# Kernel tuning notes

Measured on AMD Instinct MI355X. Metric: run time of the kernel, lower is better.

## Reference

```python
import jax, jax.numpy as jnp
import numpy as np

N = 50000
E = 800000
F_IN = 128
HID = 64
HEADS = 4
NUM_TYPES = 1
NEG_SLOPE = 0.2


def setup_inputs() -> dict:
    key = jax.random.key(0)
    ks = jax.random.split(key, 20)
    s = 0.05
    inp = {
        "node_features": jax.random.normal(ks[0], (N, F_IN), jnp.float32),
        "node_types": jax.random.randint(ks[1], (N,), 0, NUM_TYPES, jnp.int32),
        "edge_index": jax.random.randint(ks[2], (2, E), 0, N, jnp.int32),
        # params
        "type_emb": jax.random.normal(ks[3], (NUM_TYPES, HID), jnp.float32) * s,
        "proj_w": jax.random.normal(ks[4], (F_IN, HID), jnp.float32) * s,
        "proj_b": jnp.zeros((HID,), jnp.float32),
        # GAT layer 0: in=64 -> heads*64, concat=True
        "lin_w0": jax.random.normal(ks[5], (HID, HEADS * HID), jnp.float32) * s,
        "att_src0": jax.random.normal(ks[6], (HEADS, HID), jnp.float32) * s,
        "att_dst0": jax.random.normal(ks[7], (HEADS, HID), jnp.float32) * s,
        "bias0": jnp.zeros((HEADS * HID,), jnp.float32),
        "ln_g0": jnp.ones((HEADS * HID,), jnp.float32),
        "ln_b0": jnp.zeros((HEADS * HID,), jnp.float32),
        # GAT layer 1: in=256 -> heads*64, concat=False (mean over heads)
        "lin_w1": jax.random.normal(ks[8], (HEADS * HID, HEADS * HID), jnp.float32) * s,
        "att_src1": jax.random.normal(ks[9], (HEADS, HID), jnp.float32) * s,
        "att_dst1": jax.random.normal(ks[10], (HEADS, HID), jnp.float32) * s,
        "bias1": jnp.zeros((HID,), jnp.float32),
        "ln_g1": jnp.ones((HID,), jnp.float32),
        "ln_b1": jnp.zeros((HID,), jnp.float32),
    }
    return inp


def _layer_norm(x, g, b, eps=1e-5):
    mu = jnp.mean(x, axis=-1, keepdims=True)
    var = jnp.mean(jnp.square(x - mu), axis=-1, keepdims=True)
    return (x - mu) * jax.lax.rsqrt(var + eps) * g + b


def _gat_conv(x, src, dst, lin_w, att_src, att_dst, bias, concat):
    # PyG GATConv: linear -> per-edge additive attention -> segment softmax over
    # incoming edges -> weighted scatter-sum. Self-loops already in src/dst.
    n = x.shape[0]
    H, C = att_src.shape
    h = (x @ lin_w).reshape(n, H, C)            # [N,H,C]
    a_s = jnp.sum(h * att_src[None], axis=-1)   # [N,H]
    a_d = jnp.sum(h * att_dst[None], axis=-1)   # [N,H]
    a = jax.nn.leaky_relu(a_s[src] + a_d[dst], NEG_SLOPE)  # [E,H]
    m = jax.ops.segment_max(a, dst, num_segments=n)
    e = jnp.exp(a - m[dst])
    z = jax.ops.segment_sum(e, dst, num_segments=n)
    alpha = e / z[dst]                           # [E,H]
    msg = h[src] * alpha[..., None]              # [E,H,C]
    out = jax.ops.segment_sum(msg, dst, num_segments=n)  # [N,H,C]
    if concat:
        out = out.reshape(n, H * C)
    else:
        out = out.mean(axis=1)
    return out + bias


def reference(node_features, node_types, edge_index,
              type_emb, proj_w, proj_b,
              lin_w0, att_src0, att_dst0, bias0, ln_g0, ln_b0,
              lin_w1, att_src1, att_dst1, bias1, ln_g1, ln_b1):
    n = node_features.shape[0]
    # add self loops (PyG GATConv default add_self_loops=True)
    loop = jnp.arange(n, dtype=edge_index.dtype)
    src = jnp.concatenate([edge_index[0], loop])
    dst = jnp.concatenate([edge_index[1], loop])

    x = node_features @ proj_w + proj_b + type_emb[node_types]  # [N,64]

    # layer 0: no residual (i == 0)
    x = _gat_conv(x, src, dst, lin_w0, att_src0, att_dst0, bias0, concat=True)
    x = jax.nn.relu(_layer_norm(x, ln_g0, ln_b0))  # [N,256]; dropout = identity (eval)

    # layer 1: residual shape [N,256] != output [N,64] -> residual skipped
    x = _gat_conv(x, src, dst, lin_w1, att_src1, att_dst1, bias1, concat=False)
    x = jax.nn.relu(_layer_norm(x, ln_g1, ln_b1))  # [N,64]
    return x
```

## Files before the change

### kernel.cpp

```cpp
#include <hip/hip_runtime.h>


#define BLK 256
#define FB  768

typedef __bf16 bf16x8 __attribute__((ext_vector_type(8)));
typedef __bf16 bf16x4 __attribute__((ext_vector_type(4)));
typedef float  f32x4  __attribute__((ext_vector_type(4)));


__device__ __forceinline__ void pack_body(const float* __restrict__ w,
                                          __bf16* __restrict__ wp,
                                          int K, int NC, int idx) {
  const int tot = (K >> 3) * NC;
  if (idx >= tot) return;
  int g = idx / NC, c = idx - g * NC;
#pragma unroll
  for (int j = 0; j < 8; ++j)
    wp[(size_t)idx * 8 + j] = (__bf16)w[(g * 8 + j) * NC + c];
}


__global__ __launch_bounds__(BLK) void k_prep(
    const float* __restrict__ pw, const float* __restrict__ w0,
    const float* __restrict__ w1, __bf16* __restrict__ pwp,
    __bf16* __restrict__ w0p, __bf16* __restrict__ w1p,
    int* __restrict__ cnt, int* __restrict__ sidx, int n, int nchunks) {
  int b = blockIdx.x;
  const int t = threadIdx.x;
  if (b < nchunks) {
    int i = b * BLK + t;
    if (i < n) { cnt[i] = 1; sidx[(size_t)i << 6] = i; }
    return;
  }
  b -= nchunks;
  if (b < 4)  { pack_body(pw, pwp, 128, 64,  b * BLK + t); return; }
  b -= 4;
  if (b < 8)  { pack_body(w0, w0p, 64, 256,  b * BLK + t); return; }
  b -= 8;
  pack_body(w1, w1p, 256, 256, b * BLK + t);
}

__global__ __launch_bounds__(BLK) void k_fill_projlin0(
    const int* __restrict__ src, const int* __restrict__ dst,
    int* __restrict__ cnt, int* __restrict__ sidx, int E,
    const float* __restrict__ nf, const int* __restrict__ types,
    const __bf16* __restrict__ pwp, const float* __restrict__ pb,
    const float* __restrict__ emb,
    const __bf16* __restrict__ w0p,
    const float* __restrict__ asrc0, const float* __restrict__ adst0,
    __bf16* __restrict__ H, float* __restrict__ as_, float* __restrict__ ad_,
    int n) {
  __shared__ __bf16 xt[64][72];
  if (blockIdx.x < FB) {
    const int st = FB * BLK;
    for (int e = blockIdx.x * BLK + threadIdx.x; e < E; e += 4 * st) {
      const int e1 = e + st, e2 = e + 2 * st, e3 = e + 3 * st;
      const bool vB = e1 < E, vC = e2 < E, vD = e3 < E;
      int sA = src[e], dA = dst[e];
      int sB = 0, dB = 0, sC = 0, dC = 0, sD = 0, dD = 0;
      if (vB) { sB = src[e1]; dB = dst[e1]; }
      if (vC) { sC = src[e2]; dC = dst[e2]; }
      if (vD) { sD = src[e3]; dD = dst[e3]; }
      int slA = atomicAdd(&cnt[dA], 1);
      int slB = vB ? atomicAdd(&cnt[dB], 1) : 64;
      int slC = vC ? atomicAdd(&cnt[dC], 1) : 64;
      int slD = vD ? atomicAdd(&cnt[dD], 1) : 64;
      if (slA < 64) sidx[((size_t)dA << 6) + slA] = sA;
      if (slB < 64) sidx[((size_t)dB << 6) + slB] = sB;
      if (slC < 64) sidx[((size_t)dC << 6) + slC] = sC;
      if (slD < 64) sidx[((size_t)dD << 6) + slD] = sD;
    }
    return;
  }
  const int bid = blockIdx.x - FB;
  const int t = threadIdx.x, w = t >> 6, l = t & 63;
  const int l15 = l & 15, lg = l >> 4;
  const int m0 = bid * 64;

  {
    const int mbase = m0 + w * 16;
    f32x4 acc[4] = {};
    const int ar = mbase + l15;
    const bool av = ar < n;
#pragma unroll
    for (int ks = 0; ks < 4; ++ks) {
      bf16x8 a = {};
      if (av) {
        const float* ap = nf + (size_t)ar * 128 + ks * 32 + lg * 8;
        float4 f0 = *(const float4*)(ap);
        float4 f1 = *(const float4*)(ap + 4);
        a[0] = (__bf16)f0.x; a[1] = (__bf16)f0.y; a[2] = (__bf16)f0.z; a[3] = (__bf16)f0.w;
        a[4] = (__bf16)f1.x; a[5] = (__bf16)f1.y; a[6] = (__bf16)f1.z; a[7] = (__bf16)f1.w;
      }
#pragma unroll
      for (int nt = 0; nt < 4; ++nt) {
        int c = nt * 16 + l15;
        int g = ks * 4 + lg;
        bf16x8 b = *(const bf16x8*)(pwp + ((size_t)g * 64 + c) * 8);
        acc[nt] = __builtin_amdgcn_mfma_f32_16x16x32_bf16(a, b, acc[nt], 0, 0, 0);
      }
    }
#pragma unroll
    for (int reg = 0; reg < 4; ++reg) {
      int row = mbase + lg * 4 + reg;
      int lrow = w * 16 + lg * 4 + reg;
      if (row < n) {
        int ty = types[row];
#pragma unroll
        for (int nt = 0; nt < 4; ++nt) {
          int c = nt * 16 + l15;
          xt[lrow][c] = (__bf16)(acc[nt][reg] + pb[c] + emb[ty * 64 + c]);
        }
      } else {
#pragma unroll
        for (int nt = 0; nt < 4; ++nt) xt[lrow][nt * 16 + l15] = (__bf16)0.f;
      }
    }
  }
  __syncthreads();

  float asv[4], adv[4];
#pragma unroll
  for (int nt = 0; nt < 4; ++nt) {
    int c = w * 64 + nt * 16 + l15;
    asv[nt] = asrc0[c];
    adv[nt] = adst0[c];
  }
  f32x4 acc[4][4] = {};
  for (int ks = 0; ks < 2; ++ks) {
    bf16x8 a[4];
#pragma unroll
    for (int mt = 0; mt < 4; ++mt)
      a[mt] = *(const bf16x8*)&xt[mt * 16 + l15][ks * 32 + lg * 8];
    bf16x8 b[4];
#pragma unroll
    for (int nt = 0; nt < 4; ++nt) {
      int c = w * 64 + nt * 16 + l15;
      int g = ks * 4 + lg;
      b[nt] = *(const bf16x8*)(w0p + ((size_t)g * 256 + c) * 8);
    }
#pragma unroll
    for (int nt = 0; nt < 4; ++nt)
#pragma unroll
      for (int mt = 0; mt < 4; ++mt)
        acc[mt][nt] = __builtin_amdgcn_mfma_f32_16x16x32_bf16(a[mt], b[nt], acc[mt][nt], 0, 0, 0);
  }
#pragma unroll
  for (int mt = 0; mt < 4; ++mt) {
#pragma unroll
    for (int reg = 0; reg < 4; ++reg) {
      int row = m0 + mt * 16 + lg * 4 + reg;
      bool vr = row < n;
      float s = 0.f, d = 0.f;
      if (vr) {
#pragma unroll
        for (int nt = 0; nt < 4; ++nt) {
          float cv = acc[mt][nt][reg];
          H[(size_t)row * 256 + w * 64 + nt * 16 + l15] = (__bf16)cv;
          s = fmaf(cv, asv[nt], s);
          d = fmaf(cv, adv[nt], d);
        }
      }
#pragma unroll
      for (int o = 8; o; o >>= 1) { s += __shfl_xor(s, o); d += __shfl_xor(d, o); }
      if (l15 == 0 && vr) { as_[row * 4 + w] = s; ad_[row * 4 + w] = d; }
    }
  }
}

__global__ __launch_bounds__(BLK) void k_lin256(
    const __bf16* __restrict__ X, const __bf16* __restrict__ Wp,
    const float* __restrict__ att_s, const float* __restrict__ att_d,
    __bf16* __restrict__ H, float* __restrict__ as_, float* __restrict__ ad_, int n) {
  const int t = threadIdx.x, w = t >> 6, l = t & 63;
  const int l15 = l & 15, lg = l >> 4;
  const int m0 = blockIdx.x * 64;

  float asv[4], adv[4];
#pragma unroll
  for (int nt = 0; nt < 4; ++nt) {
    int c = w * 64 + nt * 16 + l15;
    asv[nt] = att_s[c];
    adv[nt] = att_d[c];
  }

  f32x4 acc[4][4] = {};
  int rr[4];
  bool vv[4];
#pragma unroll
  for (int mt = 0; mt < 4; ++mt) { rr[mt] = m0 + mt * 16 + l15; vv[mt] = rr[mt] < n; }
  const bf16x8 zf = {};

  for (int ks = 0; ks < 8; ++ks) {
    bf16x8 a[4];
#pragma unroll
    for (int mt = 0; mt < 4; ++mt)
      a[mt] = vv[mt] ? *(const bf16x8*)(X + (size_t)rr[mt] * 256 + ks * 32 + lg * 8) : zf;
    bf16x8 b[4];
#pragma unroll
    for (int nt = 0; nt < 4; ++nt) {
      int c = w * 64 + nt * 16 + l15;
      int g = ks * 4 + lg;
      b[nt] = *(const bf16x8*)(Wp + ((size_t)g * 256 + c) * 8);
    }
#pragma unroll
    for (int nt = 0; nt < 4; ++nt)
#pragma unroll
      for (int mt = 0; mt < 4; ++mt)
        acc[mt][nt] = __builtin_amdgcn_mfma_f32_16x16x32_bf16(a[mt], b[nt], acc[mt][nt], 0, 0, 0);
  }

#pragma unroll
  for (int mt = 0; mt < 4; ++mt) {
#pragma unroll
    for (int reg = 0; reg < 4; ++reg) {
      int row = m0 + mt * 16 + lg * 4 + reg;
      bool vr = row < n;
      float s = 0.f, d = 0.f;
      if (vr) {
#pragma unroll
        for (int nt = 0; nt < 4; ++nt) {
          float cv = acc[mt][nt][reg];
          H[(size_t)row * 256 + w * 64 + nt * 16 + l15] = (__bf16)cv;
          s = fmaf(cv, asv[nt], s);
          d = fmaf(cv, adv[nt], d);
        }
      }
#pragma unroll
      for (int o = 8; o; o >>= 1) { s += __shfl_xor(s, o); d += __shfl_xor(d, o); }
      if (l15 == 0 && vr) { as_[row * 4 + w] = s; ad_[row * 4 + w] = d; }
    }
  }
}


__global__ __launch_bounds__(BLK) void k_agg0(
    const int* __restrict__ cntA, const int* __restrict__ sidx,
    const float* __restrict__ as_, const float* __restrict__ ad_,
    const __bf16* __restrict__ h0,
    const float* __restrict__ bias, const float* __restrict__ g,
    const float* __restrict__ b, __bf16* __restrict__ x1, int n) {
  const int lane = threadIdx.x & 63;
  const int wid = (blockIdx.x * BLK + threadIdx.x) >> 6;
  const int nw = (gridDim.x * BLK) >> 6;
  const int hsel = lane >> 4;
  const float4 bias4 = ((const float4*)bias)[lane];
  const float4 g4 = ((const float4*)g)[lane];
  const float4 b4 = ((const float4*)b)[lane];
  for (int d = wid; d < n; d += nw) {
    int cnt = cntA[d]; if (cnt > 64) cnt = 64;
    const int* sp = sidx + ((size_t)d << 6);
    const float adv = ad_[d * 4 + hsel];
    float ax = 0.f, ay = 0.f, az = 0.f, aw = 0.f, z = 0.f;
    int j = 0;
    for (; j + 4 <= cnt; j += 4) {
      int4 s4 = *(const int4*)(sp + j);
      int s0 = __builtin_amdgcn_readfirstlane(s4.x);
      int s1 = __builtin_amdgcn_readfirstlane(s4.y);
      int s2 = __builtin_amdgcn_readfirstlane(s4.z);
      int s3 = __builtin_amdgcn_readfirstlane(s4.w);
      float q0 = as_[s0 * 4 + hsel], q1 = as_[s1 * 4 + hsel];
      float q2 = as_[s2 * 4 + hsel], q3 = as_[s3 * 4 + hsel];
      bf16x4 v0 = *(const bf16x4*)(h0 + (size_t)s0 * 256 + lane * 4);
      bf16x4 v1 = *(const bf16x4*)(h0 + (size_t)s1 * 256 + lane * 4);
      bf16x4 v2 = *(const bf16x4*)(h0 + (size_t)s2 * 256 + lane * 4);
      bf16x4 v3 = *(const bf16x4*)(h0 + (size_t)s3 * 256 + lane * 4);
      float a;
      a = q0 + adv; a = fmaxf(a, 0.2f * a); float e0 = __expf(a);
      a = q1 + adv; a = fmaxf(a, 0.2f * a); float e1 = __expf(a);
      a = q2 + adv; a = fmaxf(a, 0.2f * a); float e2 = __expf(a);
      a = q3 + adv; a = fmaxf(a, 0.2f * a); float e3 = __expf(a);
      z += (e0 + e1) + (e2 + e3);
      ax = fmaf(e0, (float)v0[0], ax); ay = fmaf(e0, (float)v0[1], ay);
      az = fmaf(e0, (float)v0[2], az); aw = fmaf(e0, (float)v0[3], aw);
      ax = fmaf(e1, (float)v1[0], ax); ay = fmaf(e1, (float)v1[1], ay);
      az = fmaf(e1, (float)v1[2], az); aw = fmaf(e1, (float)v1[3], aw);
      ax = fmaf(e2, (float)v2[0], ax); ay = fmaf(e2, (float)v2[1], ay);
      az = fmaf(e2, (float)v2[2], az); aw = fmaf(e2, (float)v2[3], aw);
      ax = fmaf(e3, (float)v3[0], ax); ay = fmaf(e3, (float)v3[1], ay);
      az = fmaf(e3, (float)v3[2], az); aw = fmaf(e3, (float)v3[3], aw);
    }
    for (; j < cnt; ++j) {
      int s = __builtin_amdgcn_readfirstlane(sp[j]);
      float a = as_[s * 4 + hsel] + adv; a = fmaxf(a, 0.2f * a);
      float e = __expf(a);
      z += e;
      bf16x4 hv = *(const bf16x4*)(h0 + (size_t)s * 256 + lane * 4);
      ax = fmaf(e, (float)hv[0], ax); ay = fmaf(e, (float)hv[1], ay);
      az = fmaf(e, (float)hv[2], az); aw = fmaf(e, (float)hv[3], aw);
    }
    float rz = 1.f / z;
    float vx = ax * rz + bias4.x, vy = ay * rz + bias4.y;
    float vz = az * rz + bias4.z, vw = aw * rz + bias4.w;
    float s1 = vx + vy + vz + vw;
#pragma unroll
    for (int o = 32; o; o >>= 1) s1 += __shfl_xor(s1, o);
    float mu = s1 * (1.f / 256.f);
    float dx = vx - mu, dy = vy - mu, dz = vz - mu, dw = vw - mu;
    float q = dx * dx + dy * dy + dz * dz + dw * dw;
#pragma unroll
    for (int o = 32; o; o >>= 1) q += __shfl_xor(q, o);
    float is = rsqrtf(q * (1.f / 256.f) + 1e-5f);
    bf16x4 o4;
    o4[0] = (__bf16)fmaxf(dx * is * g4.x + b4.x, 0.f);
    o4[1] = (__bf16)fmaxf(dy * is * g4.y + b4.y, 0.f);
    o4[2] = (__bf16)fmaxf(dz * is * g4.z + b4.z, 0.f);
    o4[3] = (__bf16)fmaxf(dw * is * g4.w + b4.w, 0.f);
    *(bf16x4*)(x1 + (size_t)d * 256 + lane * 4) = o4;
  }
}

__global__ __launch_bounds__(BLK) void k_agg1(
    const int* __restrict__ cntA, const int* __restrict__ sidx,
    const float* __restrict__ as_, const float* __restrict__ ad_,
    const __bf16* __restrict__ h1,
    const float* __restrict__ bias, const float* __restrict__ g,
    const float* __restrict__ b, float* __restrict__ out, int n) {
  const int lane = threadIdx.x & 63;
  const int wid = (blockIdx.x * BLK + threadIdx.x) >> 6;
  const int nw = (gridDim.x * BLK) >> 6;
  const int hsel = lane >> 4;
  const int p = lane & 15;
  const float4 bias4 = ((const float4*)bias)[p];
  const float4 g4 = ((const float4*)g)[p];
  const float4 b4 = ((const float4*)b)[p];
  for (int d = wid; d < n; d += nw) {
    int cnt = cntA[d]; if (cnt > 64) cnt = 64;
    const int* sp = sidx + ((size_t)d << 6);
    const float adv = ad_[d * 4 + hsel];
    float ax = 0.f, ay = 0.f, az = 0.f, aw = 0.f, z = 0.f;
    int j = 0;
    for (; j + 4 <= cnt; j += 4) {
      int4 s4 = *(const int4*)(sp + j);
      int s0 = __builtin_amdgcn_readfirstlane(s4.x);
      int s1 = __builtin_amdgcn_readfirstlane(s4.y);
      int s2 = __builtin_amdgcn_readfirstlane(s4.z);
      int s3 = __builtin_amdgcn_readfirstlane(s4.w);
      float q0 = as_[s0 * 4 + hsel], q1 = as_[s1 * 4 + hsel];
      float q2 = as_[s2 * 4 + hsel], q3 = as_[s3 * 4 + hsel];
      bf16x4 v0 = *(const bf16x4*)(h1 + (size_t)s0 * 256 + lane * 4);
      bf16x4 v1 = *(const bf16x4*)(h1 + (size_t)s1 * 256 + lane * 4);
      bf16x4 v2 = *(const bf16x4*)(h1 + (size_t)s2 * 256 + lane * 4);
      bf16x4 v3 = *(const bf16x4*)(h1 + (size_t)s3 * 256 + lane * 4);
      float a;
      a = q0 + adv; a = fmaxf(a, 0.2f * a); float e0 = __expf(a);
      a = q1 + adv; a = fmaxf(a, 0.2f * a); float e1 = __expf(a);
      a = q2 + adv; a = fmaxf(a, 0.2f * a); float e2 = __expf(a);
      a = q3 + adv; a = fmaxf(a, 0.2f * a); float e3 = __expf(a);
      z += (e0 + e1) + (e2 + e3);
      ax = fmaf(e0, (float)v0[0], ax); ay = fmaf(e0, (float)v0[1], ay);
      az = fmaf(e0, (float)v0[2], az); aw = fmaf(e0, (float)v0[3], aw);
      ax = fmaf(e1, (float)v1[0], ax); ay = fmaf(e1, (float)v1[1], ay);
      az = fmaf(e1, (float)v1[2], az); aw = fmaf(e1, (float)v1[3], aw);
      ax = fmaf(e2, (float)v2[0], ax); ay = fmaf(e2, (float)v2[1], ay);
      az = fmaf(e2, (float)v2[2], az); aw = fmaf(e2, (float)v2[3], aw);
      ax = fmaf(e3, (float)v3[0], ax); ay = fmaf(e3, (float)v3[1], ay);
      az = fmaf(e3, (float)v3[2], az); aw = fmaf(e3, (float)v3[3], aw);
    }
    for (; j < cnt; ++j) {
      int s = __builtin_amdgcn_readfirstlane(sp[j]);
      float a = as_[s * 4 + hsel] + adv; a = fmaxf(a, 0.2f * a);
      float e = __expf(a);
      z += e;
      bf16x4 hv = *(const bf16x4*)(h1 + (size_t)s * 256 + lane * 4);
      ax = fmaf(e, (float)hv[0], ax); ay = fmaf(e, (float)hv[1], ay);
      az = fmaf(e, (float)hv[2], az); aw = fmaf(e, (float)hv[3], aw);
    }
    float rz = 1.f / z;
    ax *= rz; ay *= rz; az *= rz; aw *= rz;
#pragma unroll
    for (int o = 16; o <= 32; o <<= 1) {
      ax += __shfl_xor(ax, o); ay += __shfl_xor(ay, o);
      az += __shfl_xor(az, o); aw += __shfl_xor(aw, o);
    }
    float vx = 0.25f * ax + bias4.x, vy = 0.25f * ay + bias4.y;
    float vz = 0.25f * az + bias4.z, vw = 0.25f * aw + bias4.w;
    float s1 = vx + vy + vz + vw;
#pragma unroll
    for (int o = 8; o; o >>= 1) s1 += __shfl_xor(s1, o);
    float mu = s1 * (1.f / 64.f);
    float dx = vx - mu, dy = vy - mu, dz = vz - mu, dw = vw - mu;
    float q = dx * dx + dy * dy + dz * dz + dw * dw;
#pragma unroll
    for (int o = 8; o; o >>= 1) q += __shfl_xor(q, o);
    float is = rsqrtf(q * (1.f / 64.f) + 1e-5f);
    if (lane < 16) {
      float4 o4;
      o4.x = fmaxf(dx * is * g4.x + b4.x, 0.f);
      o4.y = fmaxf(dy * is * g4.y + b4.y, 0.f);
      o4.z = fmaxf(dz * is * g4.z + b4.z, 0.f);
      o4.w = fmaxf(dw * is * g4.w + b4.w, 0.f);
      ((float4*)(out + (size_t)d * 64))[p] = o4;
    }
  }
}

extern "C" void kernel_launch(void* const* d_in, const int* in_sizes, int n_in,
                              void* d_out, int out_size, void* d_ws, size_t ws_size,
                              hipStream_t stream) {
  const float* nf    = (const float*)d_in[0];
  const int*   types = (const int*)d_in[1];
  const int*   ei    = (const int*)d_in[2];
  const float* emb   = (const float*)d_in[3];
  const float* pw    = (const float*)d_in[4];
  const float* pb    = (const float*)d_in[5];
  const float* w0    = (const float*)d_in[6];
  const float* asrc0 = (const float*)d_in[7];
  const float* adst0 = (const float*)d_in[8];
  const float* b0    = (const float*)d_in[9];
  const float* g0    = (const float*)d_in[10];
  const float* be0   = (const float*)d_in[11];
  const float* w1    = (const float*)d_in[12];
  const float* asrc1 = (const float*)d_in[13];
  const float* adst1 = (const float*)d_in[14];
  const float* b1    = (const float*)d_in[15];
  const float* g1    = (const float*)d_in[16];
  const float* be1   = (const float*)d_in[17];

  const int n = in_sizes[0] / 128;
  const int E = in_sizes[2] / 2;
  const int* srcI = ei;
  const int* dstI = ei + E;

  float* W = (float*)d_ws;
  size_t o = 0;
  __bf16* h   = (__bf16*)(W + o); o += (size_t)n * 128;
  __bf16* x1  = (__bf16*)(W + o); o += (size_t)n * 128;
  float* as_ = W + o;             o += (size_t)n * 4;
  float* ad_ = W + o;             o += (size_t)n * 4;
  __bf16* w0p = (__bf16*)(W + o); o += 64 * 256 / 2;
  __bf16* w1p = (__bf16*)(W + o); o += 256 * 256 / 2;
  __bf16* pwp = (__bf16*)(W + o); o += 128 * 64 / 2;
  int* I = (int*)(W + o);
  size_t io = 0;
  int* cnt  = I + io; io += n;
  int* sidx = I + io; io += (size_t)n * 64;

  const int nchunks = (n + BLK - 1) / BLK;
  const int mgrid = (n + 63) / 64;
  const int agrid = (n * 64 + BLK - 1) / BLK;

  k_prep<<<nchunks + 44, BLK, 0, stream>>>(pw, w0, w1, pwp, w0p, w1p, cnt, sidx, n, nchunks);
  k_fill_projlin0<<<FB + mgrid, BLK, 0, stream>>>(srcI, dstI, cnt, sidx, E,
                                                  nf, types, pwp, pb, emb,
                                                  w0p, asrc0, adst0, h, as_, ad_, n);
  k_agg0<<<agrid, BLK, 0, stream>>>(cnt, sidx, as_, ad_, h, b0, g0, be0, x1, n);
  k_lin256<<<mgrid, BLK, 0, stream>>>(x1, w1p, asrc1, adst1, h, as_, ad_, n);
  k_agg1<<<agrid, BLK, 0, stream>>>(cnt, sidx, as_, ad_, h, b1, g1, be1,
                                    (float*)d_out, n);
}
```

Baseline: 247.8 us.

## Fuse layer-0 aggregation with layer-1 linear via shared-memory tile

Merges the layer-0 attention aggregation plus LayerNorm kernel with the layer-1 256x256 linear projection. Each block aggregates 16 destination rows into a shared-memory tile, then runs MFMA on that tile directly, so the x1 intermediate is never written to or re-read from global memory and one launch is removed. The trade-off is that each block reloads the full 256x256 weight matrix for only 16 rows, and the aggregation is no longer grid-strided, which could add weight traffic and change occupancy.

```diff
diff --git a/kernel.cpp b/kernel.cpp
--- a/kernel.cpp
+++ b/kernel.cpp
@@ -40,6 +40,7 @@
   b -= 8;
   pack_body(w1, w1p, 256, 256, b * BLK + t);
 }
+
 
 __global__ __launch_bounds__(BLK) void k_fill_projlin0(
     const int* __restrict__ src, const int* __restrict__ dst,
@@ -169,147 +170,134 @@
   }
 }
 
-__global__ __launch_bounds__(BLK) void k_lin256(
-    const __bf16* __restrict__ X, const __bf16* __restrict__ Wp,
-    const float* __restrict__ att_s, const float* __restrict__ att_d,
-    __bf16* __restrict__ H, float* __restrict__ as_, float* __restrict__ ad_, int n) {
-  const int t = threadIdx.x, w = t >> 6, l = t & 63;
-  const int l15 = l & 15, lg = l >> 4;
-  const int m0 = blockIdx.x * 64;
-
+
+__global__ __launch_bounds__(BLK) void k_agg0_lin1(
+    const int* __restrict__ cntA, const int* __restrict__ sidx,
+    const float* __restrict__ as0, const float* __restrict__ ad0,
+    const __bf16* __restrict__ h0,
+    const float* __restrict__ bias, const float* __restrict__ g,
+    const float* __restrict__ b,
+    const __bf16* __restrict__ w1p,
+    const float* __restrict__ asrc1, const float* __restrict__ adst1,
+    __bf16* __restrict__ H1, float* __restrict__ as1, float* __restrict__ ad1,
+    int n) {
+  __shared__ __bf16 xt[16][264];
+  const int t = threadIdx.x, w = t >> 6, lane = t & 63;
+  const int hsel = lane >> 4, l15 = lane & 15;
+  const int gbase = blockIdx.x * 16;
+  const float4 bias4 = ((const float4*)bias)[lane];
+  const float4 g4 = ((const float4*)g)[lane];
+  const float4 b4 = ((const float4*)b)[lane];
+
+  for (int q = 0; q < 4; ++q) {
+    const int d = gbase + w * 4 + q;
+    const int lrow = w * 4 + q;
+    if (d < n) {
+      int cnt = cntA[d]; if (cnt > 64) cnt = 64;
+      const int* sp = sidx + ((size_t)d << 6);
+      const float adv = ad0[d * 4 + hsel];
+      float ax = 0.f, ay = 0.f, az = 0.f, aw = 0.f, z = 0.f;
+      int j = 0;
+      for (; j + 4 <= cnt; j += 4) {
+        int4 s4 = *(const int4*)(sp + j);
+        int s0 = __builtin_amdgcn_readfirstlane(s4.x);
+        int s1 = __builtin_amdgcn_readfirstlane(s4.y);
+        int s2 = __builtin_amdgcn_readfirstlane(s4.z);
+        int s3 = __builtin_amdgcn_readfirstlane(s4.w);
+        float q0 = as0[s0 * 4 + hsel], q1 = as0[s1 * 4 + hsel];
+        float q2 = as0[s2 * 4 + hsel], q3 = as0[s3 * 4 + hsel];
+        bf16x4 v0 = *(const bf16x4*)(h0 + (size_t)s0 * 256 + lane * 4);
+        bf16x4 v1 = *(const bf16x4*)(h0 + (size_t)s1 * 256 + lane * 4);
+        bf16x4 v2 = *(const bf16x4*)(h0 + (size_t)s2 * 256 + lane * 4);
+        bf16x4 v3 = *(const bf16x4*)(h0 + (size_t)s3 * 256 + lane * 4);
+        float a;
+        a = q0 + adv; a = fmaxf(a, 0.2f * a); float e0 = __expf(a);
+        a = q1 + adv; a = fmaxf(a, 0.2f * a); float e1 = __expf(a);
+        a = q2 + adv; a = fmaxf(a, 0.2f * a); float e2 = __expf(a);
+        a = q3 + adv; a = fmaxf(a, 0.2f * a); float e3 = __expf(a);
+        z += (e0 + e1) + (e2 + e3);
+        ax = fmaf(e0, (float)v0[0], ax); ay = fmaf(e0, (float)v0[1], ay);
+        az = fmaf(e0, (float)v0[2], az); aw = fmaf(e0, (float)v0[3], aw);
+        ax = fmaf(e1, (float)v1[0], ax); ay = fmaf(e1, (float)v1[1], ay);
+        az = fmaf(e1, (float)v1[2], az); aw = fmaf(e1, (float)v1[3], aw);
+        ax = fmaf(e2, (float)v2[0], ax); ay = fmaf(e2, (float)v2[1], ay);
+        az = fmaf(e2, (float)v2[2], az); aw = fmaf(e2, (float)v2[3], aw);
+        ax = fmaf(e3, (float)v3[0], ax); ay = fmaf(e3, (float)v3[1], ay);
+        az = fmaf(e3, (float)v3[2], az); aw = fmaf(e3, (float)v3[3], aw);
+      }
+      for (; j < cnt; ++j) {
+        int s = __builtin_amdgcn_readfirstlane(sp[j]);
+        float a = as0[s * 4 + hsel] + adv; a = fmaxf(a, 0.2f * a);
+        float e = __expf(a);
+        z += e;
+        bf16x4 hv = *(const bf16x4*)(h0 + (size_t)s * 256 + lane * 4);
+        ax = fmaf(e, (float)hv[0], ax); ay = fmaf(e, (float)hv[1], ay);
+        az = fmaf(e, (float)hv[2], az); aw = fmaf(e, (float)hv[3], aw);
+      }
+      float rz = 1.f / z;
+      float vx = ax * rz + bias4.x, vy = ay * rz + bias4.y;
+      float vz = az * rz + bias4.z, vw = aw * rz + bias4.w;
+      float s1 = vx + vy + vz + vw;
+#pragma unroll
+      for (int o = 32; o; o >>= 1) s1 += __shfl_xor(s1, o);
+      float mu = s1 * (1.f / 256.f);
+      float dx = vx - mu, dy = vy - mu, dz = vz - mu, dw = vw - mu;
+      float qq = dx * dx + dy * dy + dz * dz + dw * dw;
+#pragma unroll
+      for (int o = 32; o; o >>= 1) qq += __shfl_xor(qq, o);
+      float is = rsqrtf(qq * (1.f / 256.f) + 1e-5f);
+      bf16x4 o4;
+      o4[0] = (__bf16)fmaxf(dx * is * g4.x + b4.x, 0.f);
+      o4[1] = (__bf16)fmaxf(dy * is * g4.y + b4.y, 0.f);
+      o4[2] = (__bf16)fmaxf(dz * is * g4.z + b4.z, 0.f);
+      o4[3] = (__bf16)fmaxf(dw * is * g4.w + b4.w, 0.f);
+      *(bf16x4*)&xt[lrow][lane * 4] = o4;
+    } else {
+      bf16x4 zf = {};
+      *(bf16x4*)&xt[lrow][lane * 4] = zf;
+    }
+  }
+  __syncthreads();
+
+  const int lg = hsel;
   float asv[4], adv[4];
 #pragma unroll
   for (int nt = 0; nt < 4; ++nt) {
     int c = w * 64 + nt * 16 + l15;
-    asv[nt] = att_s[c];
-    adv[nt] = att_d[c];
-  }
-
-  f32x4 acc[4][4] = {};
-  int rr[4];
-  bool vv[4];
-#pragma unroll
-  for (int mt = 0; mt < 4; ++mt) { rr[mt] = m0 + mt * 16 + l15; vv[mt] = rr[mt] < n; }
-  const bf16x8 zf = {};
-
+    asv[nt] = asrc1[c];
+    adv[nt] = adst1[c];
+  }
+  f32x4 acc[4] = {};
   for (int ks = 0; ks < 8; ++ks) {
-    bf16x8 a[4];
-#pragma unroll
-    for (int mt = 0; mt < 4; ++mt)
-      a[mt] = vv[mt] ? *(const bf16x8*)(X + (size_t)rr[mt] * 256 + ks * 32 + lg * 8) : zf;
-    bf16x8 b[4];
+    bf16x8 a = *(const bf16x8*)&xt[l15][ks * 32 + lg * 8];
 #pragma unroll
     for (int nt = 0; nt < 4; ++nt) {
       int c = w * 64 + nt * 16 + l15;
       int g = ks * 4 + lg;
-      b[nt] = *(const bf16x8*)(Wp + ((size_t)g * 256 + c) * 8);
-    }
-#pragma unroll
-    for (int nt = 0; nt < 4; ++nt)
-#pragma unroll
-      for (int mt = 0; mt < 4; ++mt)
-        acc[mt][nt] = __builtin_amdgcn_mfma_f32_16x16x32_bf16(a[mt], b[nt], acc[mt][nt], 0, 0, 0);
-  }
-
-#pragma unroll
-  for (int mt = 0; mt < 4; ++mt) {
-#pragma unroll
-    for (int reg = 0; reg < 4; ++reg) {
-      int row = m0 + mt * 16 + lg * 4 + reg;
-      bool vr = row < n;
-      float s = 0.f, d = 0.f;
-      if (vr) {
-#pragma unroll
-        for (int nt = 0; nt < 4; ++nt) {
-          float cv = acc[mt][nt][reg];
-          H[(size_t)row * 256 + w * 64 + nt * 16 + l15] = (__bf16)cv;
-          s = fmaf(cv, asv[nt], s);
-          d = fmaf(cv, adv[nt], d);
-        }
-      }
-#pragma unroll
-      for (int o = 8; o; o >>= 1) { s += __shfl_xor(s, o); d += __shfl_xor(d, o); }
-      if (l15 == 0 && vr) { as_[row * 4 + w] = s; ad_[row * 4 + w] = d; }
-    }
-  }
-}
-
-
-__global__ __launch_bounds__(BLK) void k_agg0(
-    const int* __restrict__ cntA, const int* __restrict__ sidx,
-    const float* __restrict__ as_, const float* __restrict__ ad_,
-    const __bf16* __restrict__ h0,
-    const float* __restrict__ bias, const float* __restrict__ g,
-    const float* __restrict__ b, __bf16* __restrict__ x1, int n) {
-  const int lane = threadIdx.x & 63;
-  const int wid = (blockIdx.x * BLK + threadIdx.x) >> 6;
-  const int nw = (gridDim.x * BLK) >> 6;
-  const int hsel = lane >> 4;
-  const float4 bias4 = ((const float4*)bias)[lane];
-  const float4 g4 = ((const float4*)g)[lane];
-  const float4 b4 = ((const float4*)b)[lane];
-  for (int d = wid; d < n; d += nw) {
-    int cnt = cntA[d]; if (cnt > 64) cnt = 64;
-    const int* sp = sidx + ((size_t)d << 6);
-    const float adv = ad_[d * 4 + hsel];
-    float ax = 0.f, ay = 0.f, az = 0.f, aw = 0.f, z = 0.f;
-    int j = 0;
-    for (; j + 4 <= cnt; j += 4) {
-      int4 s4 = *(const int4*)(sp + j);
-      int s0 = __builtin_amdgcn_readfirstlane(s4.x);
-      int s1 = __builtin_amdgcn_readfirstlane(s4.y);
-      int s2 = __builtin_amdgcn_readfirstlane(s4.z);
-      int s3 = __builtin_amdgcn_readfirstlane(s4.w);
-      float q0 = as_[s0 * 4 + hsel], q1 = as_[s1 * 4 + hsel];
-      float q2 = as_[s2 * 4 + hsel], q3 = as_[s3 * 4 + hsel];
-      bf16x4 v0 = *(const bf16x4*)(h0 + (size_t)s0 * 256 + lane * 4);
-      bf16x4 v1 = *(const bf16x4*)(h0 + (size_t)s1 * 256 + lane * 4);
-      bf16x4 v2 = *(const bf16x4*)(h0 + (size_t)s2 * 256 + lane * 4);
-      bf16x4 v3 = *(const bf16x4*)(h0 + (size_t)s3 * 256 + lane * 4);
-      float a;
-      a = q0 + adv; a = fmaxf(a, 0.2f * a); float e0 = __expf(a);
-      a = q1 + adv; a = fmaxf(a, 0.2f * a); float e1 = __expf(a);
-      a = q2 + adv; a = fmaxf(a, 0.2f * a); float e2 = __expf(a);
-      a = q3 + adv; a = fmaxf(a, 0.2f * a); float e3 = __expf(a);
-      z += (e0 + e1) + (e2 + e3);
-      ax = fmaf(e0, (float)v0[0], ax); ay = fmaf(e0, (float)v0[1], ay);
-      az = fmaf(e0, (float)v0[2], az); aw = fmaf(e0, (float)v0[3], aw);
-      ax = fmaf(e1, (float)v1[0], ax); ay = fmaf(e1, (float)v1[1], ay);
-      az = fmaf(e1, (float)v1[2], az); aw = fmaf(e1, (float)v1[3], aw);
-      ax = fmaf(e2, (float)v2[0], ax); ay = fmaf(e2, (float)v2[1], ay);
-      az = fmaf(e2, (float)v2[2], az); aw = fmaf(e2, (float)v2[3], aw);
-      ax = fmaf(e3, (float)v3[0], ax); ay = fmaf(e3, (float)v3[1], ay);
-      az = fmaf(e3, (float)v3[2], az); aw = fmaf(e3, (float)v3[3], aw);
-    }
-    for (; j < cnt; ++j) {
-      int s = __builtin_amdgcn_readfirstlane(sp[j]);
-      float a = as_[s * 4 + hsel] + adv; a = fmaxf(a, 0.2f * a);
-      float e = __expf(a);
-      z += e;
-      bf16x4 hv = *(const bf16x4*)(h0 + (size_t)s * 256 + lane * 4);
-      ax = fmaf(e, (float)hv[0], ax); ay = fmaf(e, (float)hv[1], ay);
-      az = fmaf(e, (float)hv[2], az); aw = fmaf(e, (float)hv[3], aw);
-    }
-    float rz = 1.f / z;
-    float vx = ax * rz + bias4.x, vy = ay * rz + bias4.y;
-    float vz = az * rz + bias4.z, vw = aw * rz + bias4.w;
-    float s1 = vx + vy + vz + vw;
-#pragma unroll
-    for (int o = 32; o; o >>= 1) s1 += __shfl_xor(s1, o);
-    float mu = s1 * (1.f / 256.f);
-    float dx = vx - mu, dy = vy - mu, dz = vz - mu, dw = vw - mu;
-    float q = dx * dx + dy * dy + dz * dz + dw * dw;
-#pragma unroll
-    for (int o = 32; o; o >>= 1) q += __shfl_xor(q, o);
-    float is = rsqrtf(q * (1.f / 256.f) + 1e-5f);
-    bf16x4 o4;
-    o4[0] = (__bf16)fmaxf(dx * is * g4.x + b4.x, 0.f);
-    o4[1] = (__bf16)fmaxf(dy * is * g4.y + b4.y, 0.f);
-    o4[2] = (__bf16)fmaxf(dz * is * g4.z + b4.z, 0.f);
-    o4[3] = (__bf16)fmaxf(dw * is * g4.w + b4.w, 0.f);
-    *(bf16x4*)(x1 + (size_t)d * 256 + lane * 4) = o4;
-  }
-}
+      bf16x8 bb = *(const bf16x8*)(w1p + ((size_t)g * 256 + c) * 8);
+      acc[nt] = __builtin_amdgcn_mfma_f32_16x16x32_bf16(a, bb, acc[nt], 0, 0, 0);
+    }
+  }
+#pragma unroll
+  for (int reg = 0; reg < 4; ++reg) {
+    int row = gbase + lg * 4 + reg;
+    bool vr = row < n;
+    float s = 0.f, d = 0.f;
+    if (vr) {
+#pragma unroll
+      for (int nt = 0; nt < 4; ++nt) {
+        float cv = acc[nt][reg];
+        H1[(size_t)row * 256 + w * 64 + nt * 16 + l15] = (__bf16)cv;
+        s = fmaf(cv, asv[nt], s);
+        d = fmaf(cv, adv[nt], d);
+      }
+    }
+#pragma unroll
+    for (int o = 8; o; o >>= 1) { s += __shfl_xor(s, o); d += __shfl_xor(d, o); }
+    if (l15 == 0 && vr) { as1[row * 4 + w] = s; ad1[row * 4 + w] = d; }
+  }
+}
+
 
 __global__ __launch_bounds__(BLK) void k_agg1(
     const int* __restrict__ cntA, const int* __restrict__ sidx,
@@ -425,10 +413,12 @@
 
   float* W = (float*)d_ws;
   size_t o = 0;
-  __bf16* h   = (__bf16*)(W + o); o += (size_t)n * 128;
-  __bf16* x1  = (__bf16*)(W + o); o += (size_t)n * 128;
-  float* as_ = W + o;             o += (size_t)n * 4;
-  float* ad_ = W + o;             o += (size_t)n * 4;
+  __bf16* h0b = (__bf16*)(W + o); o += (size_t)n * 128;
+  __bf16* h1b = (__bf16*)(W + o); o += (size_t)n * 128;
+  float* as0 = W + o;             o += (size_t)n * 4;
+  float* ad0 = W + o;             o += (size_t)n * 4;
+  float* as1 = W + o;             o += (size_t)n * 4;
+  float* ad1 = W + o;             o += (size_t)n * 4;
   __bf16* w0p = (__bf16*)(W + o); o += 64 * 256 / 2;
   __bf16* w1p = (__bf16*)(W + o); o += 256 * 256 / 2;
   __bf16* pwp = (__bf16*)(W + o); o += 128 * 64 / 2;
@@ -439,14 +429,15 @@
 
   const int nchunks = (n + BLK - 1) / BLK;
   const int mgrid = (n + 63) / 64;
+  const int ggrid = (n + 15) / 16;
   const int agrid = (n * 64 + BLK - 1) / BLK;
 
   k_prep<<<nchunks + 44, BLK, 0, stream>>>(pw, w0, w1, pwp, w0p, w1p, cnt, sidx, n, nchunks);
   k_fill_projlin0<<<FB + mgrid, BLK, 0, stream>>>(srcI, dstI, cnt, sidx, E,
                                                   nf, types, pwp, pb, emb,
-                                                  w0p, asrc0, adst0, h, as_, ad_, n);
-  k_agg0<<<agrid, BLK, 0, stream>>>(cnt, sidx, as_, ad_, h, b0, g0, be0, x1, n);
-  k_lin256<<<mgrid, BLK, 0, stream>>>(x1, w1p, asrc1, adst1, h, as_, ad_, n);
-  k_agg1<<<agrid, BLK, 0, stream>>>(cnt, sidx, as_, ad_, h, b1, g1, be1,
+                                                  w0p, asrc0, adst0, h0b, as0, ad0, n);
+  k_agg0_lin1<<<ggrid, BLK, 0, stream>>>(cnt, sidx, as0, ad0, h0b, b0, g0, be0,
+                                         w1p, asrc1, adst1, h1b, as1, ad1, n);
+  k_agg1<<<agrid, BLK, 0, stream>>>(cnt, sidx, as1, ad1, h1b, b1, g1, be1,
                                     (float*)d_out, n);
 }
```

Result: no change. 245.6 us (-0.9%).
